# Optimization experiments

Measured on AMD Instinct MI355X. Metric: run time of the kernel, lower is better.

## Reference

```python
import jax, jax.numpy as jnp
import numpy as np

B, SQ, SKV, D, H = 2, 2048, 2048, 1024, 16
HD = D // H

def setup_inputs() -> dict:
    key = jax.random.key(0)
    ks = jax.random.split(key, 11)
    def xavier(k, shape):
        fan_in, fan_out = shape[1], shape[0]
        lim = jnp.sqrt(6.0 / (fan_in + fan_out))
        return jax.random.uniform(k, shape, jnp.float32, -lim, lim)
    return {
        'query': jax.random.normal(ks[0], (B, SQ, D), jnp.float32),
        'key': jax.random.normal(ks[1], (B, SKV, D), jnp.float32),
        'value': jax.random.normal(ks[2], (B, SKV, D), jnp.float32),
        'Wq': xavier(ks[3], (D, D)), 'bq': jnp.zeros((D,), jnp.float32),
        'Wk': xavier(ks[4], (D, D)), 'bk': jnp.zeros((D,), jnp.float32),
        'Wv': xavier(ks[5], (D, D)), 'bv': jnp.zeros((D,), jnp.float32),
        'Wo': xavier(ks[6], (D, D)), 'bo': jnp.zeros((D,), jnp.float32),
    }

def reference(query, key, value, Wq, bq, Wk, bk, Wv, bv, Wo, bo):
    # Linear uses y = x @ W.T + b (torch convention, W: [out, in])
    Q = query @ Wq.T + bq   # [B, SQ, D]
    K = key @ Wk.T + bk     # [B, SKV, D]
    V = value @ Wv.T + bv   # [B, SKV, D]
    Q = Q.reshape(B, SQ, H, HD).transpose(0, 2, 1, 3)   # [B,H,SQ,HD]
    K = K.reshape(B, SKV, H, HD).transpose(0, 2, 1, 3)  # [B,H,SKV,HD]
    V = V.reshape(B, SKV, H, HD).transpose(0, 2, 1, 3)
    scores = jnp.einsum('bhqd,bhkd->bhqk', Q, K) / jnp.sqrt(jnp.float32(HD))
    probs = jax.nn.softmax(scores, axis=-1)  # dropout is identity at eval
    ctx = jnp.einsum('bhqk,bhkd->bhqd', probs, V)
    ctx = ctx.transpose(0, 2, 1, 3).reshape(B, SQ, D)
    return ctx @ Wo.T + bo
```

## Files before the change

kernel.cpp:

```cpp
#include <hip/hip_runtime.h>

#define DIM   1024
#define NHEAD 16
#define HDIM  64
#define BATCH 2
#define SEQ   2048
#define MTOT  4096

typedef unsigned short u16;
typedef unsigned int   u32;
typedef __attribute__((ext_vector_type(8))) short bf16x8;
typedef __attribute__((ext_vector_type(4))) short u16x4;
typedef __attribute__((ext_vector_type(4))) float f32x4;
typedef __attribute__((ext_vector_type(4))) u32   u32x4;

#define QSCALE 0.18033688011112042f
#define EXP2F(x) __builtin_amdgcn_exp2f(x)

__device__ __forceinline__ void gload_lds16(const void* g, void* l) {
  __builtin_amdgcn_global_load_lds((const __attribute__((address_space(1))) void*)g,
                                   (__attribute__((address_space(3))) void*)l, 16, 0, 0);
}

__device__ __forceinline__ u16 f32_to_bf16(float f) {
  union { float f; u32 u; } v; v.f = f;
  u32 r = v.u + 0x7fffu + ((v.u >> 16) & 1u);
  return (u16)(r >> 16);
}

struct CvtArgs {
  const float* s[7];
  u16*         d[7];
  int          n8[7];
};

__global__ __launch_bounds__(256) void cvt_all(CvtArgs a) {
  const int z = blockIdx.z;
  const float* s = a.s[z];
  u16* d = a.d[z];
  const int n8 = a.n8[z];
  const int stride = gridDim.x * blockDim.x;
  for (int i = blockIdx.x * blockDim.x + threadIdx.x; i < n8; i += stride) {
    float4 x = ((const float4*)s)[2 * i], y = ((const float4*)s)[2 * i + 1];
    u16 o[8] = { f32_to_bf16(x.x), f32_to_bf16(x.y), f32_to_bf16(x.z), f32_to_bf16(x.w),
                 f32_to_bf16(y.x), f32_to_bf16(y.y), f32_to_bf16(y.z), f32_to_bf16(y.w) };
    *(u32x4*)&d[(size_t)i * 8] = *(const u32x4*)o;
  }
}

template<int MF, bool OUTF32, bool BIAS_ROW>
__device__ __forceinline__ void gemm_body(
    const u16* __restrict__ X, const u16* __restrict__ W,
    const float* __restrict__ bias, void* __restrict__ Cv, int ldc, float scale,
    int m0, int n0)
{
  __shared__ __align__(16) u16 ldsA[32 * 4 * 64];
  __shared__ __align__(16) u16 ldsB[128 * 64];
  const int tid  = threadIdx.x;
  const int lane = tid & 63;
  const int wid  = tid >> 6;
  const int wr   = wid >> 1, wc = wid & 1;
  const int srow = tid >> 3;
  const int scs  = tid & 7;

  f32x4 acc[MF][4];
#pragma unroll
  for (int mf = 0; mf < MF; ++mf)
#pragma unroll
    for (int nf = 0; nf < 4; ++nf)
#pragma unroll
      for (int r = 0; r < 4; ++r) acc[mf][nf][r] = 0.f;

  for (int kt = 0; kt < DIM; kt += 64) {
    __syncthreads();
#pragma unroll
    for (int call = 0; call < MF; ++call) {
      int row = call * 32 + srow;
      int lc  = scs ^ (row & 7);
      gload_lds16(X + (size_t)(m0 + row) * DIM + kt + lc * 8,
                  &ldsA[(row * 8 + scs) * 8]);
    }
#pragma unroll
    for (int call = 0; call < 4; ++call) {
      int row = call * 32 + srow;
      int lc  = scs ^ (row & 7);
      gload_lds16(W + (size_t)(n0 + row) * DIM + kt + lc * 8,
                  &ldsB[(row * 8 + scs) * 8]);
    }
    __syncthreads();
#pragma unroll
    for (int ks = 0; ks < 2; ++ks) {
      bf16x8 af[MF], bfr[4];
#pragma unroll
      for (int mf = 0; mf < MF; ++mf) {
        int row = wr * (16 * MF) + mf * 16 + (lane & 15);
        int ch  = (ks * 4 + (lane >> 4)) ^ (row & 7);
        af[mf] = *(const bf16x8*)&ldsA[row * 64 + ch * 8];
      }
#pragma unroll
      for (int nf = 0; nf < 4; ++nf) {
        int row = wc * 64 + nf * 16 + (lane & 15);
        int ch  = (ks * 4 + (lane >> 4)) ^ (row & 7);
        bfr[nf] = *(const bf16x8*)&ldsB[row * 64 + ch * 8];
      }
#pragma unroll
      for (int mf = 0; mf < MF; ++mf)
#pragma unroll
        for (int nf = 0; nf < 4; ++nf)
          acc[mf][nf] = __builtin_amdgcn_mfma_f32_16x16x32_bf16(
              af[mf], bfr[nf], acc[mf][nf], 0, 0, 0);
    }
  }
#pragma unroll
  for (int nf = 0; nf < 4; ++nf) {
    int col = n0 + wc * 64 + nf * 16 + (lane & 15);
    float bcol = BIAS_ROW ? 0.f : bias[col];
#pragma unroll
    for (int mf = 0; mf < MF; ++mf) {
      int rbase = m0 + wr * (16 * MF) + mf * 16 + ((lane >> 4) << 2);
#pragma unroll
      for (int r = 0; r < 4; ++r) {
        float bv = BIAS_ROW ? bias[rbase + r] : bcol;
        float v = (acc[mf][nf][r] + bv) * scale;
        if (OUTF32) ((float*)Cv)[(size_t)(rbase + r) * ldc + col] = v;
        else        ((u16*)Cv)[(size_t)(rbase + r) * ldc + col] = f32_to_bf16(v);
      }
    }
  }
}

__global__ __launch_bounds__(256, 2) void gemm_proj_kernel(
    const u16* __restrict__ q, const u16* __restrict__ k, const u16* __restrict__ v,
    const u16* __restrict__ wq, const u16* __restrict__ wk, const u16* __restrict__ wv,
    const float* __restrict__ bq, const float* __restrict__ bk, const float* __restrict__ bv,
    u16* __restrict__ oq, u16* __restrict__ ok, u16* __restrict__ ovt)
{
  const int z = blockIdx.z;
  if (z == 0)
    gemm_body<4, false, false>(q, wq, bq, oq, DIM, QSCALE,
                               blockIdx.y * 128, blockIdx.x * 128);
  else if (z == 1)
    gemm_body<4, false, false>(k, wk, bk, ok, DIM, 1.0f,
                               blockIdx.y * 128, blockIdx.x * 128);
  else
    gemm_body<4, false, true>(wv, v, bv, ovt, MTOT, 1.0f,
                              blockIdx.x * 128, blockIdx.y * 128);
}

__global__ __launch_bounds__(256, 2) void gemm_o_kernel(
    const u16* __restrict__ x, const u16* __restrict__ w,
    const float* __restrict__ b, float* __restrict__ c)
{
  gemm_body<2, true, false>(x, w, b, c, DIM, 1.0f,
                            blockIdx.y * 64, blockIdx.x * 128);
}

#define PSTR 72

__global__ __launch_bounds__(256, 2) void attn_kernel(
    const u16* __restrict__ Qm, const u16* __restrict__ Km,
    const u16* __restrict__ Vt, u16* __restrict__ Cm)
{
  __shared__ __align__(16) u16 Kl[2][64 * 64];
  __shared__ __align__(16) u16 Vl[2][64 * 64];
  __shared__ __align__(16) u16 Pl[4][32 * PSTR];

  const int tid = threadIdx.x, lane = tid & 63, wid = tid >> 6;
  const int c = lane & 15, g = lane >> 4;
  const int wkid = (blockIdx.x & 7) * 64 + (blockIdx.x >> 3);
  const int qt = wkid & 15;
  const int bh = wkid >> 4;
  const int b = bh >> 4, h = bh & 15;
  const size_t hb = (size_t)h * HDIM;
  const int q0 = qt * 128 + wid * 32;
  const u16* Qh = Qm + ((size_t)b * SEQ + q0) * DIM + hb;
  const u16* Kh = Km + (size_t)b * SEQ * DIM + hb;
  const u16* Vh = Vt + (size_t)(h * HDIM) * MTOT + (size_t)b * SEQ;

  bf16x8 qf[2][2];
#pragma unroll
  for (int mf = 0; mf < 2; ++mf)
#pragma unroll
    for (int ks = 0; ks < 2; ++ks)
      qf[mf][ks] = *(const bf16x8*)(Qh + (size_t)(16 * mf + c) * DIM + ks * 32 + g * 8);

  bf16x8 ones;
#pragma unroll
  for (int j = 0; j < 8; ++j) ((short*)&ones)[j] = (short)0x3F80;

  f32x4 oacc[2][4], lacc[2];
#pragma unroll
  for (int mf = 0; mf < 2; ++mf) {
#pragma unroll
    for (int nd = 0; nd < 4; ++nd)
#pragma unroll
      for (int r = 0; r < 4; ++r) oacc[mf][nd][r] = 0.f;
#pragma unroll
    for (int r = 0; r < 4; ++r) lacc[mf][r] = 0.f;
  }

  const int srow = tid >> 3, scs = tid & 7;
  u16* pw = &Pl[wid][0];

#define STAGE(T, BUF)                                                          \
  {                                                                            \
    const int kvs = (T) * 64;                                                  \
    _Pragma("unroll")                                                          \
    for (int call = 0; call < 2; ++call) {                                     \
      int row = call * 32 + srow;                                              \
      int lc  = scs ^ (row & 7);                                               \
      gload_lds16(Kh + (size_t)(kvs + row) * DIM + lc * 8,                     \
                  &Kl[BUF][(row * 8 + scs) * 8]);                              \
      gload_lds16(Vh + (size_t)row * MTOT + kvs + lc * 8,                      \
                  &Vl[BUF][(row * 8 + scs) * 8]);                              \
    }                                                                          \
  }

  STAGE(0, 0);

  for (int t = 0; t < 32; ++t) {
    const int cur = t & 1;
    if (t < 31) {
      STAGE(t + 1, cur ^ 1);
      asm volatile("s_waitcnt vmcnt(4)" ::: "memory");
    } else {
      asm volatile("s_waitcnt vmcnt(0)" ::: "memory");
    }
    __builtin_amdgcn_sched_barrier(0);
    __builtin_amdgcn_s_barrier();
    __builtin_amdgcn_sched_barrier(0);

    f32x4 sacc[4][2];
#pragma unroll
    for (int nvk = 0; nvk < 4; ++nvk)
#pragma unroll
      for (int mf = 0; mf < 2; ++mf)
#pragma unroll
        for (int r = 0; r < 4; ++r) sacc[nvk][mf][r] = 0.f;
#pragma unroll
    for (int ks = 0; ks < 2; ++ks) {
      bf16x8 kf[4];
#pragma unroll
      for (int nvk = 0; nvk < 4; ++nvk) {
        int row = nvk * 16 + c;
        int ch  = (ks * 4 + g) ^ (row & 7);
        kf[nvk] = *(const bf16x8*)&Kl[cur][row * 64 + ch * 8];
      }
#pragma unroll
      for (int nvk = 0; nvk < 4; ++nvk)
#pragma unroll
        for (int mf = 0; mf < 2; ++mf)
          sacc[nvk][mf] = __builtin_amdgcn_mfma_f32_16x16x32_bf16(
              kf[nvk], qf[mf][ks], sacc[nvk][mf], 0, 0, 0);
    }

#pragma unroll
    for (int nvk = 0; nvk < 4; ++nvk)
#pragma unroll
      for (int mf = 0; mf < 2; ++mf) {
        u16x4 pk;
#pragma unroll
        for (int r = 0; r < 4; ++r)
          pk[r] = (short)f32_to_bf16(EXP2F(sacc[nvk][mf][r]));
        *(u16x4*)&pw[(16 * mf + c) * PSTR + 16 * nvk + 4 * g] = pk;
      }

#pragma unroll
    for (int ks = 0; ks < 2; ++ks) {
      bf16x8 pf[2];
#pragma unroll
      for (int mf = 0; mf < 2; ++mf)
        pf[mf] = *(const bf16x8*)&pw[(16 * mf + c) * PSTR + ks * 32 + g * 8];
#pragma unroll
      for (int mf = 0; mf < 2; ++mf)
        lacc[mf] = __builtin_amdgcn_mfma_f32_16x16x32_bf16(
            pf[mf], ones, lacc[mf], 0, 0, 0);
#pragma unroll
      for (int nd = 0; nd < 4; ++nd) {
        int row = nd * 16 + c;
        int ch  = (ks * 4 + g) ^ (row & 7);
        bf16x8 vfr = *(const bf16x8*)&Vl[cur][row * 64 + ch * 8];
#pragma unroll
        for (int mf = 0; mf < 2; ++mf)
          oacc[mf][nd] = __builtin_amdgcn_mfma_f32_16x16x32_bf16(
              pf[mf], vfr, oacc[mf][nd], 0, 0, 0);
      }
    }

    __builtin_amdgcn_sched_barrier(0);
    __builtin_amdgcn_s_barrier();
  }
#undef STAGE

#pragma unroll
  for (int mf = 0; mf < 2; ++mf)
#pragma unroll
    for (int nd = 0; nd < 4; ++nd)
#pragma unroll
      for (int r = 0; r < 4; ++r) {
        int q = q0 + 16 * mf + 4 * g + r;
        float v = oacc[mf][nd][r] / lacc[mf][r];
        Cm[((size_t)b * SEQ + q) * DIM + hb + nd * 16 + c] = f32_to_bf16(v);
      }
}

extern "C" void kernel_launch(void* const* d_in, const int* in_sizes, int n_in,
                              void* d_out, int out_size, void* d_ws, size_t ws_size,
                              hipStream_t stream)
{
  const float* query = (const float*)d_in[0];
  const float* key   = (const float*)d_in[1];
  const float* value = (const float*)d_in[2];
  const float* Wq = (const float*)d_in[3];  const float* bq = (const float*)d_in[4];
  const float* Wk = (const float*)d_in[5];  const float* bk = (const float*)d_in[6];
  const float* Wv = (const float*)d_in[7];  const float* bv = (const float*)d_in[8];
  const float* Wo = (const float*)d_in[9];  const float* bo = (const float*)d_in[10];
  float* out = (float*)d_out;

  const size_t NQKV = (size_t)MTOT * DIM;
  const size_t NW   = (size_t)DIM * DIM;
  u16* base = (u16*)d_ws;
  u16* Qb  = base;
  u16* Kb  = Qb + NQKV;
  u16* Vtb = Kb + NQKV;
  u16* Cb  = Vtb + NQKV;
  u16* qc  = Cb + NQKV;
  u16* kc  = qc + NQKV;
  u16* vc  = kc + NQKV;
  u16* wqc = vc + NQKV;
  u16* wkc = wqc + NW;
  u16* wvc = wkc + NW;
  u16* woc = wvc + NW;

  CvtArgs ca;
  ca.s[0] = query; ca.s[1] = key; ca.s[2] = value;
  ca.s[3] = Wq; ca.s[4] = Wk; ca.s[5] = Wv; ca.s[6] = Wo;
  ca.d[0] = qc; ca.d[1] = kc; ca.d[2] = vc;
  ca.d[3] = wqc; ca.d[4] = wkc; ca.d[5] = wvc; ca.d[6] = woc;
  for (int i = 0; i < 3; ++i) ca.n8[i] = (int)(NQKV / 8);
  for (int i = 3; i < 7; ++i) ca.n8[i] = (int)(NW / 8);
  cvt_all<<<dim3(256, 1, 7), 256, 0, stream>>>(ca);

  dim3 blk(256);
  gemm_proj_kernel<<<dim3(DIM / 128, MTOT / 128, 3), blk, 0, stream>>>(
      qc, kc, vc, wqc, wkc, wvc, bq, bk, bv, Qb, Kb, Vtb);
  attn_kernel<<<512, blk, 0, stream>>>(Qb, Kb, Vtb, Cb);
  gemm_o_kernel<<<dim3(DIM / 128, MTOT / 64, 1), blk, 0, stream>>>(Cb, woc, bo, out);
}
```

Before: 127.0 us.

## Fuse fp32-to-bf16 activation conversion into projection GEMM loads and remap blocks for L2 locality

The separate conversion of query/key/value to bf16 is removed. The projection GEMM now reads fp32 activations directly, packs them to bf16 in registers and writes them swizzled into LDS, which avoids writing and re-reading the bf16 copies. Only the weights are still pre-converted. The GEMM grids are flattened to 1D with an XCD-aware block remap for cache locality, and the bf16 packing in attention uses 32-bit pair packing. The cost is that the fp32 loads in the GEMM go through registers instead of async global-to-LDS loads, and each activation is converted several times, once per column tile.

```diff
diff --git a/kernel.cpp b/kernel.cpp
--- a/kernel.cpp
+++ b/kernel.cpp
@@ -10,8 +10,8 @@
 typedef unsigned short u16;
 typedef unsigned int   u32;
 typedef __attribute__((ext_vector_type(8))) short bf16x8;
-typedef __attribute__((ext_vector_type(4))) short u16x4;
 typedef __attribute__((ext_vector_type(4))) float f32x4;
+typedef __attribute__((ext_vector_type(2))) u32   u32x2;
 typedef __attribute__((ext_vector_type(4))) u32   u32x4;
 
 #define QSCALE 0.18033688011112042f
@@ -28,29 +28,29 @@
   return (u16)(r >> 16);
 }
 
-struct CvtArgs {
-  const float* s[7];
-  u16*         d[7];
-  int          n8[7];
-};
-
-__global__ __launch_bounds__(256) void cvt_all(CvtArgs a) {
-  const int z = blockIdx.z;
-  const float* s = a.s[z];
-  u16* d = a.d[z];
-  const int n8 = a.n8[z];
+__device__ __forceinline__ u32 pack_bf16(float a, float b) {
+  return (u32)f32_to_bf16(a) | ((u32)f32_to_bf16(b) << 16);
+}
+
+struct CvtArgs { const float* s[4]; u16* d[4]; };
+
+__global__ __launch_bounds__(256) void cvt_w(CvtArgs a) {
+  const float* s = a.s[blockIdx.z];
+  u16* d = a.d[blockIdx.z];
+  const int n8 = (int)((size_t)DIM * DIM / 8);
   const int stride = gridDim.x * blockDim.x;
   for (int i = blockIdx.x * blockDim.x + threadIdx.x; i < n8; i += stride) {
     float4 x = ((const float4*)s)[2 * i], y = ((const float4*)s)[2 * i + 1];
-    u16 o[8] = { f32_to_bf16(x.x), f32_to_bf16(x.y), f32_to_bf16(x.z), f32_to_bf16(x.w),
-                 f32_to_bf16(y.x), f32_to_bf16(y.y), f32_to_bf16(y.z), f32_to_bf16(y.w) };
-    *(u32x4*)&d[(size_t)i * 8] = *(const u32x4*)o;
-  }
-}
-
-template<int MF, bool OUTF32, bool BIAS_ROW>
+    u32x4 o;
+    o[0] = pack_bf16(x.x, x.y); o[1] = pack_bf16(x.z, x.w);
+    o[2] = pack_bf16(y.x, y.y); o[3] = pack_bf16(y.z, y.w);
+    *(u32x4*)&d[(size_t)i * 8] = o;
+  }
+}
+
+template<int MF, bool AF32, bool BF32, bool OUTF32, bool BIAS_ROW>
 __device__ __forceinline__ void gemm_body(
-    const u16* __restrict__ X, const u16* __restrict__ W,
+    const void* __restrict__ Xv, const void* __restrict__ Wv,
     const float* __restrict__ bias, void* __restrict__ Cv, int ldc, float scale,
     int m0, int n0)
 {
@@ -76,16 +76,38 @@
 #pragma unroll
     for (int call = 0; call < MF; ++call) {
       int row = call * 32 + srow;
-      int lc  = scs ^ (row & 7);
-      gload_lds16(X + (size_t)(m0 + row) * DIM + kt + lc * 8,
-                  &ldsA[(row * 8 + scs) * 8]);
+      if (AF32) {
+        const float* X = (const float*)Xv;
+        const float* src = X + (size_t)(m0 + row) * DIM + kt + scs * 8;
+        float4 x = *(const float4*)src, y = *(const float4*)(src + 4);
+        u32x4 o;
+        o[0] = pack_bf16(x.x, x.y); o[1] = pack_bf16(x.z, x.w);
+        o[2] = pack_bf16(y.x, y.y); o[3] = pack_bf16(y.z, y.w);
+        *(u32x4*)&ldsA[(row * 8 + (scs ^ (row & 7))) * 8] = o;
+      } else {
+        const u16* X = (const u16*)Xv;
+        int lc = scs ^ (row & 7);
+        gload_lds16(X + (size_t)(m0 + row) * DIM + kt + lc * 8,
+                    &ldsA[(row * 8 + scs) * 8]);
+      }
     }
 #pragma unroll
     for (int call = 0; call < 4; ++call) {
       int row = call * 32 + srow;
-      int lc  = scs ^ (row & 7);
-      gload_lds16(W + (size_t)(n0 + row) * DIM + kt + lc * 8,
-                  &ldsB[(row * 8 + scs) * 8]);
+      if (BF32) {
+        const float* W = (const float*)Wv;
+        const float* src = W + (size_t)(n0 + row) * DIM + kt + scs * 8;
+        float4 x = *(const float4*)src, y = *(const float4*)(src + 4);
+        u32x4 o;
+        o[0] = pack_bf16(x.x, x.y); o[1] = pack_bf16(x.z, x.w);
+        o[2] = pack_bf16(y.x, y.y); o[3] = pack_bf16(y.z, y.w);
+        *(u32x4*)&ldsB[(row * 8 + (scs ^ (row & 7))) * 8] = o;
+      } else {
+        const u16* W = (const u16*)Wv;
+        int lc = scs ^ (row & 7);
+        gload_lds16(W + (size_t)(n0 + row) * DIM + kt + lc * 8,
+                    &ldsB[(row * 8 + scs) * 8]);
+      }
     }
     __syncthreads();
 #pragma unroll
@@ -130,29 +152,35 @@
 }
 
 __global__ __launch_bounds__(256, 2) void gemm_proj_kernel(
-    const u16* __restrict__ q, const u16* __restrict__ k, const u16* __restrict__ v,
+    const float* __restrict__ q, const float* __restrict__ k, const float* __restrict__ v,
     const u16* __restrict__ wq, const u16* __restrict__ wk, const u16* __restrict__ wv,
     const float* __restrict__ bq, const float* __restrict__ bk, const float* __restrict__ bv,
     u16* __restrict__ oq, u16* __restrict__ ok, u16* __restrict__ ovt)
 {
-  const int z = blockIdx.z;
+  const int bid = blockIdx.x;
+  const int wk_ = (bid & 7) * 96 + (bid >> 3);
+  const int z = wk_ >> 8, rem = wk_ & 255;
+  const int ty = rem >> 3, tx = rem & 7;
   if (z == 0)
-    gemm_body<4, false, false>(q, wq, bq, oq, DIM, QSCALE,
-                               blockIdx.y * 128, blockIdx.x * 128);
+    gemm_body<4, true, false, false, false>(q, wq, bq, oq, DIM, QSCALE,
+                                            ty * 128, tx * 128);
   else if (z == 1)
-    gemm_body<4, false, false>(k, wk, bk, ok, DIM, 1.0f,
-                               blockIdx.y * 128, blockIdx.x * 128);
+    gemm_body<4, true, false, false, false>(k, wk, bk, ok, DIM, 1.0f,
+                                            ty * 128, tx * 128);
   else
-    gemm_body<4, false, true>(wv, v, bv, ovt, MTOT, 1.0f,
-                              blockIdx.x * 128, blockIdx.y * 128);
+    gemm_body<4, false, true, false, true>(wv, v, bv, ovt, MTOT, 1.0f,
+                                           tx * 128, ty * 128);
 }
 
 __global__ __launch_bounds__(256, 2) void gemm_o_kernel(
     const u16* __restrict__ x, const u16* __restrict__ w,
     const float* __restrict__ b, float* __restrict__ c)
 {
-  gemm_body<2, true, false>(x, w, b, c, DIM, 1.0f,
-                            blockIdx.y * 64, blockIdx.x * 128);
+  const int bid = blockIdx.x;
+  const int wk_ = (bid & 7) * 64 + (bid >> 3);
+  const int ty = wk_ >> 3, tx = wk_ & 7;
+  gemm_body<2, false, false, true, false>(x, w, b, c, DIM, 1.0f,
+                                          ty * 64, tx * 128);
 }
 
 #define PSTR 72
@@ -258,11 +286,10 @@
     for (int nvk = 0; nvk < 4; ++nvk)
 #pragma unroll
       for (int mf = 0; mf < 2; ++mf) {
-        u16x4 pk;
-#pragma unroll
-        for (int r = 0; r < 4; ++r)
-          pk[r] = (short)f32_to_bf16(EXP2F(sacc[nvk][mf][r]));
-        *(u16x4*)&pw[(16 * mf + c) * PSTR + 16 * nvk + 4 * g] = pk;
+        u32x2 pk2;
+        pk2[0] = pack_bf16(EXP2F(sacc[nvk][mf][0]), EXP2F(sacc[nvk][mf][1]));
+        pk2[1] = pack_bf16(EXP2F(sacc[nvk][mf][2]), EXP2F(sacc[nvk][mf][3]));
+        *(u32x2*)&pw[(16 * mf + c) * PSTR + 16 * nvk + 4 * g] = pk2;
       }
 
 #pragma unroll
@@ -324,26 +351,19 @@
   u16* Kb  = Qb + NQKV;
   u16* Vtb = Kb + NQKV;
   u16* Cb  = Vtb + NQKV;
-  u16* qc  = Cb + NQKV;
-  u16* kc  = qc + NQKV;
-  u16* vc  = kc + NQKV;
-  u16* wqc = vc + NQKV;
+  u16* wqc = Cb + NQKV;
   u16* wkc = wqc + NW;
   u16* wvc = wkc + NW;
   u16* woc = wvc + NW;
 
   CvtArgs ca;
-  ca.s[0] = query; ca.s[1] = key; ca.s[2] = value;
-  ca.s[3] = Wq; ca.s[4] = Wk; ca.s[5] = Wv; ca.s[6] = Wo;
-  ca.d[0] = qc; ca.d[1] = kc; ca.d[2] = vc;
-  ca.d[3] = wqc; ca.d[4] = wkc; ca.d[5] = wvc; ca.d[6] = woc;
-  for (int i = 0; i < 3; ++i) ca.n8[i] = (int)(NQKV / 8);
-  for (int i = 3; i < 7; ++i) ca.n8[i] = (int)(NW / 8);
-  cvt_all<<<dim3(256, 1, 7), 256, 0, stream>>>(ca);
+  ca.s[0] = Wq; ca.s[1] = Wk; ca.s[2] = Wv; ca.s[3] = Wo;
+  ca.d[0] = wqc; ca.d[1] = wkc; ca.d[2] = wvc; ca.d[3] = woc;
+  cvt_w<<<dim3(128, 1, 4), 256, 0, stream>>>(ca);
 
   dim3 blk(256);
-  gemm_proj_kernel<<<dim3(DIM / 128, MTOT / 128, 3), blk, 0, stream>>>(
-      qc, kc, vc, wqc, wkc, wvc, bq, bk, bv, Qb, Kb, Vtb);
+  gemm_proj_kernel<<<768, blk, 0, stream>>>(
+      query, key, value, wqc, wkc, wvc, bq, bk, bv, Qb, Kb, Vtb);
   attn_kernel<<<512, blk, 0, stream>>>(Qb, Kb, Vtb, Cb);
-  gemm_o_kernel<<<dim3(DIM / 128, MTOT / 64, 1), blk, 0, stream>>>(Cb, woc, bo, out);
-}
+  gemm_o_kernel<<<512, blk, 0, stream>>>(Cb, woc, bo, out);
+}
```

After: 129.5 us. Within noise of the previous version (+1.9%).

## Enlarge attention query tile per wave and remap GEMM block order for locality

Applied to the files above, without the earlier changes.

Each attention wave now handles 64 query rows instead of 32, so every K/V tile loaded into LDS is reused by twice as many rows. The grid shrinks to 256 blocks and launch bounds drop to one block per CU. The projection and output GEMMs switch to 1D grids with an XCD-aware block remap meant to improve L2 locality. bf16 packing is rewritten to build 32-bit pairs directly. The trade-off is higher register pressure, lower occupancy, and only 256 attention blocks to spread across the GPU.

```diff
diff --git a/kernel.cpp b/kernel.cpp
--- a/kernel.cpp
+++ b/kernel.cpp
@@ -10,8 +10,8 @@
 typedef unsigned short u16;
 typedef unsigned int   u32;
 typedef __attribute__((ext_vector_type(8))) short bf16x8;
-typedef __attribute__((ext_vector_type(4))) short u16x4;
 typedef __attribute__((ext_vector_type(4))) float f32x4;
+typedef __attribute__((ext_vector_type(2))) u32   u32x2;
 typedef __attribute__((ext_vector_type(4))) u32   u32x4;
 
 #define QSCALE 0.18033688011112042f
@@ -26,6 +26,10 @@
   union { float f; u32 u; } v; v.f = f;
   u32 r = v.u + 0x7fffu + ((v.u >> 16) & 1u);
   return (u16)(r >> 16);
+}
+
+__device__ __forceinline__ u32 pack_bf16(float a, float b) {
+  return (u32)f32_to_bf16(a) | ((u32)f32_to_bf16(b) << 16);
 }
 
 struct CvtArgs {
@@ -42,9 +46,10 @@
   const int stride = gridDim.x * blockDim.x;
   for (int i = blockIdx.x * blockDim.x + threadIdx.x; i < n8; i += stride) {
     float4 x = ((const float4*)s)[2 * i], y = ((const float4*)s)[2 * i + 1];
-    u16 o[8] = { f32_to_bf16(x.x), f32_to_bf16(x.y), f32_to_bf16(x.z), f32_to_bf16(x.w),
-                 f32_to_bf16(y.x), f32_to_bf16(y.y), f32_to_bf16(y.z), f32_to_bf16(y.w) };
-    *(u32x4*)&d[(size_t)i * 8] = *(const u32x4*)o;
+    u32x4 o;
+    o[0] = pack_bf16(x.x, x.y); o[1] = pack_bf16(x.z, x.w);
+    o[2] = pack_bf16(y.x, y.y); o[3] = pack_bf16(y.z, y.w);
+    *(u32x4*)&d[(size_t)i * 8] = o;
   }
 }
 
@@ -135,51 +140,53 @@
     const float* __restrict__ bq, const float* __restrict__ bk, const float* __restrict__ bv,
     u16* __restrict__ oq, u16* __restrict__ ok, u16* __restrict__ ovt)
 {
-  const int z = blockIdx.z;
+  const int bid = blockIdx.x;
+  const int wk_ = (bid & 7) * 96 + (bid >> 3);
+  const int z = wk_ >> 8, rem = wk_ & 255;
+  const int ty = rem >> 3, tx = rem & 7;
   if (z == 0)
-    gemm_body<4, false, false>(q, wq, bq, oq, DIM, QSCALE,
-                               blockIdx.y * 128, blockIdx.x * 128);
+    gemm_body<4, false, false>(q, wq, bq, oq, DIM, QSCALE, ty * 128, tx * 128);
   else if (z == 1)
-    gemm_body<4, false, false>(k, wk, bk, ok, DIM, 1.0f,
-                               blockIdx.y * 128, blockIdx.x * 128);
+    gemm_body<4, false, false>(k, wk, bk, ok, DIM, 1.0f, ty * 128, tx * 128);
   else
-    gemm_body<4, false, true>(wv, v, bv, ovt, MTOT, 1.0f,
-                              blockIdx.x * 128, blockIdx.y * 128);
+    gemm_body<4, false, true>(wv, v, bv, ovt, MTOT, 1.0f, tx * 128, ty * 128);
 }
 
 __global__ __launch_bounds__(256, 2) void gemm_o_kernel(
     const u16* __restrict__ x, const u16* __restrict__ w,
     const float* __restrict__ b, float* __restrict__ c)
 {
-  gemm_body<2, true, false>(x, w, b, c, DIM, 1.0f,
-                            blockIdx.y * 64, blockIdx.x * 128);
+  const int bid = blockIdx.x;
+  const int wk_ = (bid & 7) * 64 + (bid >> 3);
+  const int ty = wk_ >> 3, tx = wk_ & 7;
+  gemm_body<2, true, false>(x, w, b, c, DIM, 1.0f, ty * 64, tx * 128);
 }
 
 #define PSTR 72
 
-__global__ __launch_bounds__(256, 2) void attn_kernel(
+__global__ __launch_bounds__(256, 1) void attn_kernel(
     const u16* __restrict__ Qm, const u16* __restrict__ Km,
     const u16* __restrict__ Vt, u16* __restrict__ Cm)
 {
   __shared__ __align__(16) u16 Kl[2][64 * 64];
   __shared__ __align__(16) u16 Vl[2][64 * 64];
-  __shared__ __align__(16) u16 Pl[4][32 * PSTR];
+  __shared__ __align__(16) u16 Pl[4][64 * PSTR];
 
   const int tid = threadIdx.x, lane = tid & 63, wid = tid >> 6;
   const int c = lane & 15, g = lane >> 4;
-  const int wkid = (blockIdx.x & 7) * 64 + (blockIdx.x >> 3);
-  const int qt = wkid & 15;
-  const int bh = wkid >> 4;
+  const int wkid = (blockIdx.x & 7) * 32 + (blockIdx.x >> 3);
+  const int qt = wkid & 7;
+  const int bh = wkid >> 3;
   const int b = bh >> 4, h = bh & 15;
   const size_t hb = (size_t)h * HDIM;
-  const int q0 = qt * 128 + wid * 32;
+  const int q0 = qt * 256 + wid * 64;
   const u16* Qh = Qm + ((size_t)b * SEQ + q0) * DIM + hb;
   const u16* Kh = Km + (size_t)b * SEQ * DIM + hb;
   const u16* Vh = Vt + (size_t)(h * HDIM) * MTOT + (size_t)b * SEQ;
 
-  bf16x8 qf[2][2];
-#pragma unroll
-  for (int mf = 0; mf < 2; ++mf)
+  bf16x8 qf[4][2];
+#pragma unroll
+  for (int mf = 0; mf < 4; ++mf)
 #pragma unroll
     for (int ks = 0; ks < 2; ++ks)
       qf[mf][ks] = *(const bf16x8*)(Qh + (size_t)(16 * mf + c) * DIM + ks * 32 + g * 8);
@@ -188,9 +195,9 @@
 #pragma unroll
   for (int j = 0; j < 8; ++j) ((short*)&ones)[j] = (short)0x3F80;
 
-  f32x4 oacc[2][4], lacc[2];
-#pragma unroll
-  for (int mf = 0; mf < 2; ++mf) {
+  f32x4 oacc[4][4], lacc[4];
+#pragma unroll
+  for (int mf = 0; mf < 4; ++mf) {
 #pragma unroll
     for (int nd = 0; nd < 4; ++nd)
 #pragma unroll
@@ -230,11 +237,11 @@
     __builtin_amdgcn_s_barrier();
     __builtin_amdgcn_sched_barrier(0);
 
-    f32x4 sacc[4][2];
+    f32x4 sacc[4][4];
 #pragma unroll
     for (int nvk = 0; nvk < 4; ++nvk)
 #pragma unroll
-      for (int mf = 0; mf < 2; ++mf)
+      for (int mf = 0; mf < 4; ++mf)
 #pragma unroll
         for (int r = 0; r < 4; ++r) sacc[nvk][mf][r] = 0.f;
 #pragma unroll
@@ -249,7 +256,7 @@
 #pragma unroll
       for (int nvk = 0; nvk < 4; ++nvk)
 #pragma unroll
-        for (int mf = 0; mf < 2; ++mf)
+        for (int mf = 0; mf < 4; ++mf)
           sacc[nvk][mf] = __builtin_amdgcn_mfma_f32_16x16x32_bf16(
               kf[nvk], qf[mf][ks], sacc[nvk][mf], 0, 0, 0);
     }
@@ -257,22 +264,21 @@
 #pragma unroll
     for (int nvk = 0; nvk < 4; ++nvk)
 #pragma unroll
-      for (int mf = 0; mf < 2; ++mf) {
-        u16x4 pk;
-#pragma unroll
-        for (int r = 0; r < 4; ++r)
-          pk[r] = (short)f32_to_bf16(EXP2F(sacc[nvk][mf][r]));
-        *(u16x4*)&pw[(16 * mf + c) * PSTR + 16 * nvk + 4 * g] = pk;
+      for (int mf = 0; mf < 4; ++mf) {
+        u32x2 pk2;
+        pk2[0] = pack_bf16(EXP2F(sacc[nvk][mf][0]), EXP2F(sacc[nvk][mf][1]));
+        pk2[1] = pack_bf16(EXP2F(sacc[nvk][mf][2]), EXP2F(sacc[nvk][mf][3]));
+        *(u32x2*)&pw[(16 * mf + c) * PSTR + 16 * nvk + 4 * g] = pk2;
       }
 
 #pragma unroll
     for (int ks = 0; ks < 2; ++ks) {
-      bf16x8 pf[2];
-#pragma unroll
-      for (int mf = 0; mf < 2; ++mf)
+      bf16x8 pf[4];
+#pragma unroll
+      for (int mf = 0; mf < 4; ++mf)
         pf[mf] = *(const bf16x8*)&pw[(16 * mf + c) * PSTR + ks * 32 + g * 8];
 #pragma unroll
-      for (int mf = 0; mf < 2; ++mf)
+      for (int mf = 0; mf < 4; ++mf)
         lacc[mf] = __builtin_amdgcn_mfma_f32_16x16x32_bf16(
             pf[mf], ones, lacc[mf], 0, 0, 0);
 #pragma unroll
@@ -281,7 +287,7 @@
         int ch  = (ks * 4 + g) ^ (row & 7);
         bf16x8 vfr = *(const bf16x8*)&Vl[cur][row * 64 + ch * 8];
 #pragma unroll
-        for (int mf = 0; mf < 2; ++mf)
+        for (int mf = 0; mf < 4; ++mf)
           oacc[mf][nd] = __builtin_amdgcn_mfma_f32_16x16x32_bf16(
               pf[mf], vfr, oacc[mf][nd], 0, 0, 0);
       }
@@ -293,7 +299,7 @@
 #undef STAGE
 
 #pragma unroll
-  for (int mf = 0; mf < 2; ++mf)
+  for (int mf = 0; mf < 4; ++mf)
 #pragma unroll
     for (int nd = 0; nd < 4; ++nd)
 #pragma unroll
@@ -342,8 +348,8 @@
   cvt_all<<<dim3(256, 1, 7), 256, 0, stream>>>(ca);
 
   dim3 blk(256);
-  gemm_proj_kernel<<<dim3(DIM / 128, MTOT / 128, 3), blk, 0, stream>>>(
+  gemm_proj_kernel<<<768, blk, 0, stream>>>(
       qc, kc, vc, wqc, wkc, wvc, bq, bk, bv, Qb, Kb, Vtb);
-  attn_kernel<<<512, blk, 0, stream>>>(Qb, Kb, Vtb, Cb);
-  gemm_o_kernel<<<dim3(DIM / 128, MTOT / 64, 1), blk, 0, stream>>>(Cb, woc, bo, out);
-}
+  attn_kernel<<<256, blk, 0, stream>>>(Qb, Kb, Vtb, Cb);
+  gemm_o_kernel<<<512, blk, 0, stream>>>(Cb, woc, bo, out);
+}
```

New measurement: 142.8 us. +12.4%, slower.
